# Performance work log

Measured on AMD Instinct MI355X. Metric: run time of the kernel, lower is better.

The kernel has to match this reference:

```python
import jax, jax.numpy as jnp
import numpy as np

EMB = 512       # emb_dim
H = 8           # n_heads
HD = EMB // H   # head_dim = 64
FREQ = 64       # freq_features
PERIOD = 0.1
N = 2048


def setup_inputs() -> dict:
    key = jax.random.key(0)
    ks = jax.random.split(key, 6)
    x = jax.random.normal(ks[0], (1, N, EMB), dtype=jnp.float32)
    v = jax.random.normal(ks[1], (1, N, 3), dtype=jnp.float32)
    vec_map = v / jnp.linalg.norm(v, axis=-1, keepdims=True)  # unit direction vectors
    s_in = 1.0 / np.sqrt(EMB)
    W_qkv = jax.random.normal(ks[2], (EMB, 3 * EMB), dtype=jnp.float32) * s_in
    b_qkv = jnp.zeros((3 * EMB,), dtype=jnp.float32)
    W_bias = jax.random.normal(ks[3], (FREQ, H), dtype=jnp.float32) * (1.0 / np.sqrt(FREQ))
    b_bias = jnp.zeros((H,), dtype=jnp.float32)
    W_out = jax.random.normal(ks[4], (EMB, EMB), dtype=jnp.float32) * s_in
    b_out = jnp.zeros((EMB,), dtype=jnp.float32)
    return {"x": x, "vec_map": vec_map, "W_qkv": W_qkv, "b_qkv": b_qkv,
            "W_bias": W_bias, "b_bias": b_bias, "W_out": W_out, "b_out": b_out}


def reference(x, vec_map, W_qkv, b_qkv, W_bias, b_bias, W_out, b_out):
    batch_dim = x.shape[:-2]
    n = x.shape[-2]
    # QKV projection -> (*, N, H, 3, HD)
    qkv = (x @ W_qkv + b_qkv).reshape(*batch_dim, n, H, 3, HD)
    q, k, v = (qkv[..., 0, :], qkv[..., 1, :], qkv[..., 2, :])
    # attention scores (*, Q, K, H), softmax over the K axis (axis=-2)
    attn = jnp.einsum('...qht,...kht->...qkh', q, k) / np.sqrt(HD)
    attn = jax.nn.softmax(attn, axis=-2)
    # relative bias from pairwise angles between direction vectors
    dot = jnp.einsum('...nc,...mc->...nm', vec_map, vec_map)
    angle = jnp.arccos(jnp.clip(dot, 0.0, 1.0)) / 0.001
    freqs = jnp.linspace(0.0, 1.0, FREQ // 2, dtype=jnp.float32) / PERIOD
    phase = freqs * angle[..., None]                      # (*, N, N, FREQ/2)
    pos = jnp.concatenate((jnp.sin(phase), jnp.cos(phase)), axis=-1)  # (*, N, N, FREQ)
    bias = pos @ W_bias + b_bias                          # (*, N, N, H)
    attn = attn + bias
    # weighted sum of values -> (*, N, EMB)
    y = jnp.einsum('...qkh,...kht->...qht', attn, v).reshape(*batch_dim, n, EMB)
    return y @ W_out + b_out
```

## Files before the change

### kernel.cpp

```cpp
#include <hip/hip_runtime.h>
#include <hip/hip_bf16.h>
#include <math.h>

#define NT 2048
#define EMBD 512
#define NH 8
#define QKV_LD 1536

typedef unsigned short u16;
typedef __attribute__((ext_vector_type(8))) short short8;
typedef __attribute__((ext_vector_type(4))) float v4f;

static __device__ __forceinline__ float bf2f(unsigned int u) {
    union { unsigned int i; float f; } c; c.i = u << 16; return c.f;
}
static __device__ __forceinline__ unsigned int f2bf(float x) {
    union { float f; unsigned int u; } c; c.f = x;
    return (c.u + 0x7fffu + ((c.u >> 16) & 1u)) >> 16;
}

static __device__ __forceinline__ void split_wt_tile(const float* __restrict__ W,
    u16* __restrict__ wth, u16* __restrict__ wtl, int ld, int n0, int k0, int t)
{
    __shared__ float tile[64][65];
    const int r = t >> 2, c4 = (t & 3) << 4;
#pragma unroll
    for (int j = 0; j < 4; ++j)
        *(float4*)&tile[r][c4 + (j << 2)] =
            *(const float4*)(W + (size_t)(k0 + r) * ld + n0 + c4 + (j << 2));
    __syncthreads();
    const int n_l = t >> 2;
    u16 th[16], tl[16];
#pragma unroll
    for (int j = 0; j < 16; ++j) {
        float f = tile[c4 + j][n_l];
        unsigned int h = f2bf(f);
        th[j] = (u16)h;
        tl[j] = (u16)f2bf(f - bf2f(h));
    }
    u16* dh = wth + (size_t)(n0 + n_l) * EMBD + k0 + c4;
    u16* dl = wtl + (size_t)(n0 + n_l) * EMBD + k0 + c4;
    *(uint4*)dh       = *(uint4*)&th[0];
    *(uint4*)(dh + 8) = *(uint4*)&th[8];
    *(uint4*)dl       = *(uint4*)&tl[0];
    *(uint4*)(dl + 8) = *(uint4*)&tl[8];
}

__global__ __launch_bounds__(256) void prep(const float* __restrict__ x,
    const float* __restrict__ Wqkv, const float* __restrict__ Wout,
    u16* __restrict__ xh, u16* __restrict__ xl,
    u16* __restrict__ wth, u16* __restrict__ wtl,
    u16* __restrict__ woth, u16* __restrict__ wotl)
{
    const int b = blockIdx.x, t = threadIdx.x;
    if (b < 1024) {
        int i = (b * 256 + t) << 2;
        float4 v = *(const float4*)(x + i);
        float f[4] = {v.x, v.y, v.z, v.w};
        unsigned int hi[4], lo[4];
#pragma unroll
        for (int j = 0; j < 4; ++j) {
            hi[j] = f2bf(f[j]);
            lo[j] = f2bf(f[j] - bf2f(hi[j]));
        }
        uint2 wh; wh.x = hi[0] | (hi[1] << 16); wh.y = hi[2] | (hi[3] << 16);
        uint2 wl; wl.x = lo[0] | (lo[1] << 16); wl.y = lo[2] | (lo[3] << 16);
        *(uint2*)(xh + i) = wh;
        *(uint2*)(xl + i) = wl;
    } else if (b < 1216) {
        int bb = b - 1024;
        split_wt_tile(Wqkv, wth, wtl, QKV_LD, (bb % 24) << 6, (bb / 24) << 6, t);
    } else {
        int bb = b - 1216;
        split_wt_tile(Wout, woth, wotl, EMBD, (bb & 7) << 6, (bb >> 3) << 6, t);
    }
}

__global__ __launch_bounds__(256) void gemm_qkv_mfma(const u16* __restrict__ xh,
    const u16* __restrict__ xl, const u16* __restrict__ wth,
    const u16* __restrict__ wtl, const float* __restrict__ bias,
    u16* __restrict__ qkvb, u16* __restrict__ Vt)
{
    __shared__ u16 vtile[64][72];
    const int bn = blockIdx.x;
    const int n0 = bn << 6, m0 = blockIdx.y << 6;
    const int t = threadIdx.x;
    const int w = t >> 6, lane = t & 63;
    const int wm = w >> 1, wn = w & 1;
    const int fr = lane & 15, kd = (lane >> 4) << 3;

    const u16* ah0 = xh + (size_t)(m0 + wm * 32 + fr) * EMBD + kd;
    const u16* al0 = xl + (size_t)(m0 + wm * 32 + fr) * EMBD + kd;
    const u16* bh0 = wth + (size_t)(n0 + wn * 32 + fr) * EMBD + kd;
    const u16* bl0 = wtl + (size_t)(n0 + wn * 32 + fr) * EMBD + kd;

    v4f acc[2][2] = {};
    for (int kc = 0; kc < EMBD; kc += 32) {
        short8 a_h[2], a_l[2], b_h[2], b_l[2];
#pragma unroll
        for (int im = 0; im < 2; ++im) {
            a_h[im] = *(const short8*)(ah0 + (size_t)im * 16 * EMBD + kc);
            a_l[im] = *(const short8*)(al0 + (size_t)im * 16 * EMBD + kc);
        }
#pragma unroll
        for (int in = 0; in < 2; ++in) {
            b_h[in] = *(const short8*)(bh0 + (size_t)in * 16 * EMBD + kc);
            b_l[in] = *(const short8*)(bl0 + (size_t)in * 16 * EMBD + kc);
        }
#pragma unroll
        for (int im = 0; im < 2; ++im)
#pragma unroll
            for (int in = 0; in < 2; ++in) {
                acc[im][in] = __builtin_amdgcn_mfma_f32_16x16x32_bf16(a_h[im], b_h[in], acc[im][in], 0, 0, 0);
                acc[im][in] = __builtin_amdgcn_mfma_f32_16x16x32_bf16(a_h[im], b_l[in], acc[im][in], 0, 0, 0);
                acc[im][in] = __builtin_amdgcn_mfma_f32_16x16x32_bf16(a_l[im], b_h[in], acc[im][in], 0, 0, 0);
            }
    }
    const int qr = (lane >> 4) << 2;
    if (bn % 3 != 2) {
#pragma unroll
        for (int im = 0; im < 2; ++im)
#pragma unroll
            for (int in = 0; in < 2; ++in) {
                int n = n0 + wn * 32 + in * 16 + fr;
                float bv = bias[n];
#pragma unroll
                for (int r = 0; r < 4; ++r) {
                    int m = m0 + wm * 32 + im * 16 + qr + r;
                    qkvb[(size_t)m * QKV_LD + n] = (u16)f2bf(acc[im][in][r] + bv);
                }
            }
    } else {
        const int h = bn / 3;
#pragma unroll
        for (int im = 0; im < 2; ++im)
#pragma unroll
            for (int in = 0; in < 2; ++in) {
                int nl = wn * 32 + in * 16 + fr;
                float bv = bias[n0 + nl];
#pragma unroll
                for (int r = 0; r < 4; ++r)
                    vtile[wm * 32 + im * 16 + qr + r][nl] =
                        (u16)f2bf(acc[im][in][r] + bv);
            }
        __syncthreads();
        const int c = t >> 2, kg = (t & 3) << 4;
        u16 tmp[16];
#pragma unroll
        for (int j = 0; j < 16; ++j) tmp[j] = vtile[kg + j][c];
        u16* dst = Vt + ((size_t)h * 64 + c) * NT + m0 + kg;
        *(uint4*)dst       = *(uint4*)&tmp[0];
        *(uint4*)(dst + 8) = *(uint4*)&tmp[8];
    }
}

__global__ __launch_bounds__(256) void bias_mat(const float* __restrict__ vec,
    const float* __restrict__ Wb, const float* __restrict__ bb,
    u16* __restrict__ bm)
{
    __shared__ float flds[32];
    __shared__ float vql[96], vkl[96];
    __shared__ float bbl[8];
    __shared__ float ang_lds[1057];
    __shared__ u16 biaslu[8 * 1057];

    const int t = threadIdx.x;
    int b = blockIdx.x, tq = 0, rem = 64;
    while (b >= rem) { b -= rem; ++tq; --rem; }
    const int tk = tq + b;
    const int q0 = tq << 5, k0 = tk << 5;

    if (t < 32) flds[t] = __fdiv_rn(__fdiv_rn((float)t, 31.0f), 0.1f);
    else if (t < 128) vql[t - 32] = vec[q0 * 3 + (t - 32)];
    else if (t < 224) vkl[t - 128] = vec[k0 * 3 + (t - 128)];
    else if (t < 232) bbl[t - 224] = bb[t - 224];
    __syncthreads();

    {
        const int qq = t & 31, kb = (t >> 5) << 2;
        const float a0 = vql[qq * 3], a1 = vql[qq * 3 + 1], a2 = vql[qq * 3 + 2];
#pragma unroll
        for (int j = 0; j < 4; ++j) {
            const int kk = kb + j;
            float c0 = vkl[kk * 3], c1 = vkl[kk * 3 + 1], c2 = vkl[kk * 3 + 2];
            float dot = __fadd_rn(__fadd_rn(__fmul_rn(a0, c0), __fmul_rn(a1, c1)),
                                  __fmul_rn(a2, c2));
            float dotc = fminf(fmaxf(dot, 0.0f), 1.0f);
            ang_lds[qq * 33 + kk] = __fdiv_rn(acosf(dotc), 0.001f);
        }
    }
    __syncthreads();

    {
        const int w = t >> 6, lane = t & 63;
        const int fr = lane & 15, kd = (lane >> 4) << 3, qr = (lane >> 4) << 2;
        short8 BS, BC;
#pragma unroll
        for (int j = 0; j < 8; ++j) {
            float ws = (fr < 8) ? Wb[(kd + j) * 8 + fr] : 0.0f;
            float wc = (fr < 8) ? Wb[(32 + kd + j) * 8 + fr] : 0.0f;
            BS[j] = (short)f2bf(ws);
            BC[j] = (short)f2bf(wc);
        }
        const float bb0 = (fr < 8) ? bbl[fr] : 0.0f;
        for (int tt = w; tt < 64; tt += 4) {
            int p = (tt << 4) + fr;
            float ang = ang_lds[(p >> 5) * 33 + (p & 31)];
            short8 AS, AC;
#pragma unroll
            for (int j = 0; j < 8; ++j) {
                float ph = __fmul_rn(flds[kd + j], ang);
                float rv = ph * 0.15915494309189535f;
                float rf = rv - floorf(rv);
                AS[j] = (short)f2bf(__builtin_amdgcn_sinf(rf));
                AC[j] = (short)f2bf(__builtin_amdgcn_cosf(rf));
            }
            v4f c = {bb0, bb0, bb0, bb0};
            c = __builtin_amdgcn_mfma_f32_16x16x32_bf16(AS, BS, c, 0, 0, 0);
            c = __builtin_amdgcn_mfma_f32_16x16x32_bf16(AC, BC, c, 0, 0, 0);
            if (fr < 8) {
#pragma unroll
                for (int r = 0; r < 4; ++r) {
                    int pp = (tt << 4) + qr + r;
                    biaslu[fr * 1057 + (pp >> 5) * 33 + (pp & 31)] = (u16)f2bf(c[r]);
                }
            }
        }
    }
    __syncthreads();

    const int row = t >> 3, c4 = (t & 7) << 2;
#pragma unroll
    for (int h = 0; h < 8; ++h) {
        unsigned int o[4];
#pragma unroll
        for (int j = 0; j < 4; ++j)
            o[j] = biaslu[h * 1057 + row * 33 + c4 + j];
        uint2 wv; wv.x = o[0] | (o[1] << 16); wv.y = o[2] | (o[3] << 16);
        *(uint2*)(bm + ((size_t)h * NT + q0 + row) * NT + k0 + c4) = wv;
    }
    if (tk != tq) {
#pragma unroll
        for (int h = 0; h < 8; ++h) {
            unsigned int o[4];
#pragma unroll
            for (int j = 0; j < 4; ++j)
                o[j] = biaslu[h * 1057 + (c4 + j) * 33 + row];
            uint2 wv; wv.x = o[0] | (o[1] << 16); wv.y = o[2] | (o[3] << 16);
            *(uint2*)(bm + ((size_t)h * NT + k0 + row) * NT + q0 + c4) = wv;
        }
    }
}

__global__ __launch_bounds__(256) void biasv_mfma(const u16* __restrict__ bm,
    const u16* __restrict__ Vt, float* __restrict__ bpart)
{
    const int h = blockIdx.y, z = blockIdx.z;
    const int q0 = (blockIdx.x << 6) + ((threadIdx.x >> 6) << 4);
    const int lane = threadIdx.x & 63;
    const int fr = lane & 15;
    const int kd = (lane >> 4) << 3;
    const int kbase = z << 9;

    const u16* arow  = bm + (size_t)(h * NT + q0 + fr) * NT + kbase + kd;
    const u16* vbase = Vt + ((size_t)h * 64 + fr) * NT + kbase + kd;

    v4f c[4] = {};
    for (int ks = 0; ks < 512; ks += 64) {
        short8 a0 = *(const short8*)(arow + ks);
        short8 a1 = *(const short8*)(arow + ks + 32);
#pragma unroll
        for (int nt = 0; nt < 4; ++nt) {
            short8 b0 = *(const short8*)(vbase + (size_t)nt * 16 * NT + ks);
            short8 b1 = *(const short8*)(vbase + (size_t)nt * 16 * NT + ks + 32);
            c[nt] = __builtin_amdgcn_mfma_f32_16x16x32_bf16(a0, b0, c[nt], 0, 0, 0);
            c[nt] = __builtin_amdgcn_mfma_f32_16x16x32_bf16(a1, b1, c[nt], 0, 0, 0);
        }
    }
    float* bp = bpart + (size_t)z * NT * EMBD;
    const int qr = (lane >> 4) << 2;
#pragma unroll
    for (int nt = 0; nt < 4; ++nt)
#pragma unroll
        for (int r = 0; r < 4; ++r)
            bp[(size_t)(q0 + qr + r) * EMBD + (h << 6) + (nt << 4) + fr] = c[nt][r];
}

__global__ __launch_bounds__(256) void flash_attn(const u16* __restrict__ qkvb,
    const u16* __restrict__ Vt, u16* __restrict__ nump,
    float* __restrict__ zpart)
{
    __shared__ u16 P[4][2][16][40];
    const int h = blockIdx.y, z = blockIdx.z;
    const int w = threadIdx.x >> 6, lane = threadIdx.x & 63;
    const int fr = lane & 15, kd = (lane >> 4) << 3, qr = (lane >> 4) << 2;
    const int q0 = (blockIdx.x << 6) + (w << 4);
    const int kbase = z << 9;

    const u16* qb = qkvb + (size_t)(q0 + fr) * QKV_LD + h * 192 + kd;
    short8 qa0 = *(const short8*)(qb);
    short8 qa1 = *(const short8*)(qb + 32);
    const u16* kbp = qkvb + (size_t)kbase * QKV_LD + h * 192 + 64 + kd;
    const u16* vb  = Vt + ((size_t)h * 64 + fr) * NT + kbase + kd;

    v4f acc[4] = {};
    float zac[4] = {};
    int buf = 0;
    for (int kt = 0; kt < 512; kt += 32) {
#pragma unroll
        for (int ks = 0; ks < 2; ++ks) {
            const u16* kr = kbp + (size_t)(kt + ks * 16 + fr) * QKV_LD;
            short8 kb0 = *(const short8*)(kr);
            short8 kb1 = *(const short8*)(kr + 32);
            v4f c = {};
            c = __builtin_amdgcn_mfma_f32_16x16x32_bf16(qa0, kb0, c, 0, 0, 0);
            c = __builtin_amdgcn_mfma_f32_16x16x32_bf16(qa1, kb1, c, 0, 0, 0);
#pragma unroll
            for (int r = 0; r < 4; ++r) {
                float ex = __expf(c[r] * 0.125f);
                zac[r] += ex;
                P[w][buf][qr + r][ks * 16 + fr] = (u16)f2bf(ex);
            }
        }
        union { uint2 u2[2]; short8 s8; } pa;
        pa.u2[0] = *(uint2*)&P[w][buf][fr][kd];
        pa.u2[1] = *(uint2*)&P[w][buf][fr][kd + 4];
#pragma unroll
        for (int ti = 0; ti < 4; ++ti) {
            short8 bfr = *(const short8*)(vb + (size_t)(ti * 16) * NT + kt);
            acc[ti] = __builtin_amdgcn_mfma_f32_16x16x32_bf16(pa.s8, bfr, acc[ti], 0, 0, 0);
        }
        buf ^= 1;
    }
#pragma unroll
    for (int off = 1; off < 16; off <<= 1)
#pragma unroll
        for (int r = 0; r < 4; ++r) zac[r] += __shfl_xor(zac[r], off);
    if (fr == 0) {
#pragma unroll
        for (int r = 0; r < 4; ++r)
            zpart[((size_t)z * NH + h) * NT + q0 + qr + r] = zac[r];
    }
    u16* np = nump + (size_t)z * NT * EMBD;
#pragma unroll
    for (int ti = 0; ti < 4; ++ti)
#pragma unroll
        for (int r = 0; r < 4; ++r)
            np[(size_t)(q0 + qr + r) * EMBD + (h << 6) + (ti << 4) + fr] =
                (u16)f2bf(acc[ti][r]);
}

__global__ __launch_bounds__(256) void combine_emit(const u16* __restrict__ nump,
    const float* __restrict__ zpart, const float* __restrict__ bpart,
    u16* __restrict__ yh, u16* __restrict__ yl)
{
    const int MN = NT * EMBD;
    int i = (blockIdx.x * 256 + threadIdx.x) << 2;
    const int q = i >> 9, h = (i & 511) >> 6;
    float zs = 0.f;
#pragma unroll
    for (int z = 0; z < 4; ++z) zs += zpart[((size_t)z * NH + h) * NT + q];
    const float inv = 1.0f / zs;
    float a[4] = {};
#pragma unroll
    for (int z = 0; z < 4; ++z) {
        uint2 r = *(const uint2*)(nump + (size_t)z * MN + i);
        a[0] += bf2f(r.x & 0xffffu); a[1] += bf2f(r.x >> 16);
        a[2] += bf2f(r.y & 0xffffu); a[3] += bf2f(r.y >> 16);
    }
    float bsum[4] = {};
#pragma unroll
    for (int z = 0; z < 4; ++z) {
        float4 p = *(const float4*)(bpart + (size_t)z * MN + i);
        bsum[0] += p.x; bsum[1] += p.y; bsum[2] += p.z; bsum[3] += p.w;
    }
    unsigned int hi[4], lo[4];
#pragma unroll
    for (int j = 0; j < 4; ++j) {
        float y = a[j] * inv + bsum[j];
        hi[j] = f2bf(y);
        lo[j] = f2bf(y - bf2f(hi[j]));
    }
    uint2 wh; wh.x = hi[0] | (hi[1] << 16); wh.y = hi[2] | (hi[3] << 16);
    uint2 wl; wl.x = lo[0] | (lo[1] << 16); wl.y = lo[2] | (lo[3] << 16);
    *(uint2*)(yh + i) = wh;
    *(uint2*)(yl + i) = wl;
}

__global__ __launch_bounds__(256) void gemm_out_mfma(const u16* __restrict__ yh,
    const u16* __restrict__ yl, const u16* __restrict__ wh,
    const u16* __restrict__ wl, const float* __restrict__ bias,
    float* __restrict__ out)
{
    const int n0 = blockIdx.x << 6, m0 = blockIdx.y << 6;
    const int w = threadIdx.x >> 6, lane = threadIdx.x & 63;
    const int wm = w >> 1, wn = w & 1;
    const int fr = lane & 15, kd = (lane >> 4) << 3;

    const u16* ah0 = yh + (size_t)(m0 + wm * 32 + fr) * EMBD + kd;
    const u16* al0 = yl + (size_t)(m0 + wm * 32 + fr) * EMBD + kd;
    const u16* bh0 = wh + (size_t)(n0 + wn * 32 + fr) * EMBD + kd;
    const u16* bl0 = wl + (size_t)(n0 + wn * 32 + fr) * EMBD + kd;

    v4f acc[2][2] = {};
    for (int kc = 0; kc < EMBD; kc += 32) {
        short8 a_h[2], a_l[2], b_h[2], b_l[2];
#pragma unroll
        for (int im = 0; im < 2; ++im) {
            a_h[im] = *(const short8*)(ah0 + (size_t)im * 16 * EMBD + kc);
            a_l[im] = *(const short8*)(al0 + (size_t)im * 16 * EMBD + kc);
        }
#pragma unroll
        for (int in = 0; in < 2; ++in) {
            b_h[in] = *(const short8*)(bh0 + (size_t)in * 16 * EMBD + kc);
            b_l[in] = *(const short8*)(bl0 + (size_t)in * 16 * EMBD + kc);
        }
#pragma unroll
        for (int im = 0; im < 2; ++im)
#pragma unroll
            for (int in = 0; in < 2; ++in) {
                acc[im][in] = __builtin_amdgcn_mfma_f32_16x16x32_bf16(a_h[im], b_h[in], acc[im][in], 0, 0, 0);
                acc[im][in] = __builtin_amdgcn_mfma_f32_16x16x32_bf16(a_h[im], b_l[in], acc[im][in], 0, 0, 0);
                acc[im][in] = __builtin_amdgcn_mfma_f32_16x16x32_bf16(a_l[im], b_h[in], acc[im][in], 0, 0, 0);
            }
    }
    const int qr = (lane >> 4) << 2;
#pragma unroll
    for (int im = 0; im < 2; ++im)
#pragma unroll
        for (int in = 0; in < 2; ++in) {
            int n = n0 + wn * 32 + in * 16 + fr;
            float bv = bias[n];
#pragma unroll
            for (int r = 0; r < 4; ++r) {
                int m = m0 + wm * 32 + im * 16 + qr + r;
                out[(size_t)m * EMBD + n] = acc[im][in][r] + bv;
            }
        }
}

extern "C" void kernel_launch(void* const* d_in, const int* in_sizes, int n_in,
                              void* d_out, int out_size, void* d_ws, size_t ws_size,
                              hipStream_t stream)
{
    const float* x    = (const float*)d_in[0];
    const float* vec  = (const float*)d_in[1];
    const float* Wqkv = (const float*)d_in[2];
    const float* bqkv = (const float*)d_in[3];
    const float* Wb   = (const float*)d_in[4];
    const float* bb   = (const float*)d_in[5];
    const float* Wout = (const float*)d_in[6];
    const float* bout = (const float*)d_in[7];
    float* out = (float*)d_out;

    char* ws = (char*)d_ws;
    u16*   qkvb  = (u16*)(ws);
    u16*   Vt    = (u16*)(ws + 6291456);
    float* zpart = (float*)(ws + 8388608);
    float* bpart = (float*)(ws + 8650752);
    u16*   yh    = (u16*)(ws + 25427968);
    u16*   yl    = (u16*)(ws + 27525120);
    u16*   woth  = (u16*)(ws + 29622272);
    u16*   wotl  = (u16*)(ws + 30146560);
    char*  big   = ws + 30670848;
    u16*   xh    = (u16*)(big);
    u16*   xl    = (u16*)(big + 2097152);
    u16*   wth   = (u16*)(big + 4194304);
    u16*   wtl   = (u16*)(big + 5767168);
    u16*   bm    = (u16*)(big);
    u16*   nump  = (u16*)(big);

    prep<<<1280, 256, 0, stream>>>(x, Wqkv, Wout, xh, xl, wth, wtl, woth, wotl);
    gemm_qkv_mfma<<<dim3(24, 32), 256, 0, stream>>>(xh, xl, wth, wtl, bqkv, qkvb, Vt);
    bias_mat<<<2080, 256, 0, stream>>>(vec, Wb, bb, bm);
    biasv_mfma<<<dim3(32, 8, 4), 256, 0, stream>>>(bm, Vt, bpart);
    flash_attn<<<dim3(32, 8, 4), 256, 0, stream>>>(qkvb, Vt, nump, zpart);
    combine_emit<<<1024, 256, 0, stream>>>(nump, zpart, bpart, yh, yl);
    gemm_out_mfma<<<dim3(8, 32), 256, 0, stream>>>(yh, yl, woth, wotl, bout, out);
}
```

Baseline: 281.9 us.

## Merge bias generation into prep and fuse attention with bias-V into one launch

Folds the bias-matrix kernel into the prep kernel as extra blocks, and merges flash attention and the bias·V GEMM into a single heterogeneous launch. The bias·V part now splits K into 2 chunks instead of 4, and combine_emit sums 2 partials. The attention loop processes 64 keys per iteration with K and V loads hoisted. The workspace layout is reshuffled so bm no longer aliases the transient buffers. The aim is fewer launches, better overlap of independent work, and less partial-sum traffic, at the cost of fewer, longer bias·V blocks and a larger shared-memory footprint in the prep kernel.

```diff
diff --git a/kernel.cpp b/kernel.cpp
--- a/kernel.cpp
+++ b/kernel.cpp
@@ -20,9 +20,9 @@
 }
 
 static __device__ __forceinline__ void split_wt_tile(const float* __restrict__ W,
-    u16* __restrict__ wth, u16* __restrict__ wtl, int ld, int n0, int k0, int t)
-{
-    __shared__ float tile[64][65];
+    u16* __restrict__ wth, u16* __restrict__ wtl, int ld, int n0, int k0, int t,
+    float (*tile)[65])
+{
     const int r = t >> 2, c4 = (t & 3) << 4;
 #pragma unroll
     for (int j = 0; j < 4; ++j)
@@ -46,12 +46,16 @@
     *(uint4*)(dl + 8) = *(uint4*)&tl[8];
 }
 
-__global__ __launch_bounds__(256) void prep(const float* __restrict__ x,
+__global__ __launch_bounds__(256) void prep_bias(const float* __restrict__ x,
     const float* __restrict__ Wqkv, const float* __restrict__ Wout,
+    const float* __restrict__ vec, const float* __restrict__ Wb,
+    const float* __restrict__ bb,
     u16* __restrict__ xh, u16* __restrict__ xl,
     u16* __restrict__ wth, u16* __restrict__ wtl,
-    u16* __restrict__ woth, u16* __restrict__ wotl)
-{
+    u16* __restrict__ woth, u16* __restrict__ wotl,
+    u16* __restrict__ bm)
+{
+    __shared__ __align__(16) char smem[22080];
     const int b = blockIdx.x, t = threadIdx.x;
     if (b < 1024) {
         int i = (b * 256 + t) << 2;
@@ -67,12 +71,111 @@
         uint2 wl; wl.x = lo[0] | (lo[1] << 16); wl.y = lo[2] | (lo[3] << 16);
         *(uint2*)(xh + i) = wh;
         *(uint2*)(xl + i) = wl;
-    } else if (b < 1216) {
-        int bb = b - 1024;
-        split_wt_tile(Wqkv, wth, wtl, QKV_LD, (bb % 24) << 6, (bb / 24) << 6, t);
-    } else {
-        int bb = b - 1216;
-        split_wt_tile(Wout, woth, wotl, EMBD, (bb & 7) << 6, (bb >> 3) << 6, t);
+        return;
+    }
+    if (b < 1216) {
+        int bb2 = b - 1024;
+        split_wt_tile(Wqkv, wth, wtl, QKV_LD, (bb2 % 24) << 6, (bb2 / 24) << 6,
+                      t, (float(*)[65])smem);
+        return;
+    }
+    if (b < 1280) {
+        int bb2 = b - 1216;
+        split_wt_tile(Wout, woth, wotl, EMBD, (bb2 & 7) << 6, (bb2 >> 3) << 6,
+                      t, (float(*)[65])smem);
+        return;
+    }
+    float* flds   = (float*)(smem);
+    float* vql    = (float*)(smem + 128);
+    float* vkl    = (float*)(smem + 512);
+    float* bbl    = (float*)(smem + 896);
+    float* ang    = (float*)(smem + 928);
+    u16*   biaslu = (u16*)(smem + 5156);
+
+    int bi = b - 1280, tq = 0, rem = 64;
+    while (bi >= rem) { bi -= rem; ++tq; --rem; }
+    const int tk = tq + bi;
+    const int q0 = tq << 5, k0 = tk << 5;
+
+    if (t < 32) flds[t] = __fdiv_rn(__fdiv_rn((float)t, 31.0f), 0.1f);
+    else if (t < 128) vql[t - 32] = vec[q0 * 3 + (t - 32)];
+    else if (t < 224) vkl[t - 128] = vec[k0 * 3 + (t - 128)];
+    else if (t < 232) bbl[t - 224] = bb[t - 224];
+    __syncthreads();
+
+    {
+        const int qq = t & 31, kb = (t >> 5) << 2;
+        const float a0 = vql[qq * 3], a1 = vql[qq * 3 + 1], a2 = vql[qq * 3 + 2];
+#pragma unroll
+        for (int j = 0; j < 4; ++j) {
+            const int kk = kb + j;
+            float c0 = vkl[kk * 3], c1 = vkl[kk * 3 + 1], c2 = vkl[kk * 3 + 2];
+            float dot = __fadd_rn(__fadd_rn(__fmul_rn(a0, c0), __fmul_rn(a1, c1)),
+                                  __fmul_rn(a2, c2));
+            float dotc = fminf(fmaxf(dot, 0.0f), 1.0f);
+            ang[qq * 33 + kk] = __fdiv_rn(acosf(dotc), 0.001f);
+        }
+    }
+    __syncthreads();
+
+    {
+        const int w = t >> 6, lane = t & 63;
+        const int fr = lane & 15, kd = (lane >> 4) << 3, qr = (lane >> 4) << 2;
+        short8 BS, BC;
+#pragma unroll
+        for (int j = 0; j < 8; ++j) {
+            float ws = (fr < 8) ? Wb[(kd + j) * 8 + fr] : 0.0f;
+            float wc = (fr < 8) ? Wb[(32 + kd + j) * 8 + fr] : 0.0f;
+            BS[j] = (short)f2bf(ws);
+            BC[j] = (short)f2bf(wc);
+        }
+        const float bb0 = (fr < 8) ? bbl[fr] : 0.0f;
+        for (int tt = w; tt < 64; tt += 4) {
+            int p = (tt << 4) + fr;
+            float angv = ang[(p >> 5) * 33 + (p & 31)];
+            short8 AS, AC;
+#pragma unroll
+            for (int j = 0; j < 8; ++j) {
+                float ph = __fmul_rn(flds[kd + j], angv);
+                float rv = ph * 0.15915494309189535f;
+                float rf = rv - floorf(rv);
+                AS[j] = (short)f2bf(__builtin_amdgcn_sinf(rf));
+                AC[j] = (short)f2bf(__builtin_amdgcn_cosf(rf));
+            }
+            v4f c = {bb0, bb0, bb0, bb0};
+            c = __builtin_amdgcn_mfma_f32_16x16x32_bf16(AS, BS, c, 0, 0, 0);
+            c = __builtin_amdgcn_mfma_f32_16x16x32_bf16(AC, BC, c, 0, 0, 0);
+            if (fr < 8) {
+#pragma unroll
+                for (int r = 0; r < 4; ++r) {
+                    int pp = (tt << 4) + qr + r;
+                    biaslu[fr * 1057 + (pp >> 5) * 33 + (pp & 31)] = (u16)f2bf(c[r]);
+                }
+            }
+        }
+    }
+    __syncthreads();
+
+    const int row = t >> 3, c4 = (t & 7) << 2;
+#pragma unroll
+    for (int h = 0; h < 8; ++h) {
+        unsigned int o[4];
+#pragma unroll
+        for (int j = 0; j < 4; ++j)
+            o[j] = biaslu[h * 1057 + row * 33 + c4 + j];
+        uint2 wv; wv.x = o[0] | (o[1] << 16); wv.y = o[2] | (o[3] << 16);
+        *(uint2*)(bm + ((size_t)h * NT + q0 + row) * NT + k0 + c4) = wv;
+    }
+    if (tk != tq) {
+#pragma unroll
+        for (int h = 0; h < 8; ++h) {
+            unsigned int o[4];
+#pragma unroll
+            for (int j = 0; j < 4; ++j)
+                o[j] = biaslu[h * 1057 + (c4 + j) * 33 + row];
+            uint2 wv; wv.x = o[0] | (o[1] << 16); wv.y = o[2] | (o[3] << 16);
+            *(uint2*)(bm + ((size_t)h * NT + k0 + row) * NT + q0 + c4) = wv;
+        }
     }
 }
 
@@ -154,200 +257,113 @@
     }
 }
 
-__global__ __launch_bounds__(256) void bias_mat(const float* __restrict__ vec,
-    const float* __restrict__ Wb, const float* __restrict__ bb,
-    u16* __restrict__ bm)
-{
-    __shared__ float flds[32];
-    __shared__ float vql[96], vkl[96];
-    __shared__ float bbl[8];
-    __shared__ float ang_lds[1057];
-    __shared__ u16 biaslu[8 * 1057];
-
-    const int t = threadIdx.x;
-    int b = blockIdx.x, tq = 0, rem = 64;
-    while (b >= rem) { b -= rem; ++tq; --rem; }
-    const int tk = tq + b;
-    const int q0 = tq << 5, k0 = tk << 5;
-
-    if (t < 32) flds[t] = __fdiv_rn(__fdiv_rn((float)t, 31.0f), 0.1f);
-    else if (t < 128) vql[t - 32] = vec[q0 * 3 + (t - 32)];
-    else if (t < 224) vkl[t - 128] = vec[k0 * 3 + (t - 128)];
-    else if (t < 232) bbl[t - 224] = bb[t - 224];
-    __syncthreads();
-
-    {
-        const int qq = t & 31, kb = (t >> 5) << 2;
-        const float a0 = vql[qq * 3], a1 = vql[qq * 3 + 1], a2 = vql[qq * 3 + 2];
-#pragma unroll
-        for (int j = 0; j < 4; ++j) {
-            const int kk = kb + j;
-            float c0 = vkl[kk * 3], c1 = vkl[kk * 3 + 1], c2 = vkl[kk * 3 + 2];
-            float dot = __fadd_rn(__fadd_rn(__fmul_rn(a0, c0), __fmul_rn(a1, c1)),
-                                  __fmul_rn(a2, c2));
-            float dotc = fminf(fmaxf(dot, 0.0f), 1.0f);
-            ang_lds[qq * 33 + kk] = __fdiv_rn(acosf(dotc), 0.001f);
-        }
-    }
-    __syncthreads();
-
-    {
-        const int w = t >> 6, lane = t & 63;
-        const int fr = lane & 15, kd = (lane >> 4) << 3, qr = (lane >> 4) << 2;
-        short8 BS, BC;
-#pragma unroll
-        for (int j = 0; j < 8; ++j) {
-            float ws = (fr < 8) ? Wb[(kd + j) * 8 + fr] : 0.0f;
-            float wc = (fr < 8) ? Wb[(32 + kd + j) * 8 + fr] : 0.0f;
-            BS[j] = (short)f2bf(ws);
-            BC[j] = (short)f2bf(wc);
-        }
-        const float bb0 = (fr < 8) ? bbl[fr] : 0.0f;
-        for (int tt = w; tt < 64; tt += 4) {
-            int p = (tt << 4) + fr;
-            float ang = ang_lds[(p >> 5) * 33 + (p & 31)];
-            short8 AS, AC;
-#pragma unroll
-            for (int j = 0; j < 8; ++j) {
-                float ph = __fmul_rn(flds[kd + j], ang);
-                float rv = ph * 0.15915494309189535f;
-                float rf = rv - floorf(rv);
-                AS[j] = (short)f2bf(__builtin_amdgcn_sinf(rf));
-                AC[j] = (short)f2bf(__builtin_amdgcn_cosf(rf));
-            }
-            v4f c = {bb0, bb0, bb0, bb0};
-            c = __builtin_amdgcn_mfma_f32_16x16x32_bf16(AS, BS, c, 0, 0, 0);
-            c = __builtin_amdgcn_mfma_f32_16x16x32_bf16(AC, BC, c, 0, 0, 0);
-            if (fr < 8) {
+__global__ __launch_bounds__(256) void attn_fused(const u16* __restrict__ qkvb,
+    const u16* __restrict__ Vt, const u16* __restrict__ bm,
+    u16* __restrict__ nump, float* __restrict__ zpart,
+    float* __restrict__ bpart)
+{
+    __shared__ u16 P[4][2][16][40];
+    const int b = blockIdx.x, t = threadIdx.x;
+    const int w = t >> 6, lane = t & 63;
+    const int fr = lane & 15, kd = (lane >> 4) << 3, qr = (lane >> 4) << 2;
+    if (b < 1024) {
+        const int qb = b & 31, h = (b >> 5) & 7, z = b >> 8;
+        const int q0 = (qb << 6) + (w << 4);
+        const int kbase = z << 9;
+
+        const u16* qbp = qkvb + (size_t)(q0 + fr) * QKV_LD + h * 192 + kd;
+        short8 qa0 = *(const short8*)(qbp);
+        short8 qa1 = *(const short8*)(qbp + 32);
+        const u16* kbp = qkvb + (size_t)kbase * QKV_LD + h * 192 + 64 + kd;
+        const u16* vb  = Vt + ((size_t)h * 64 + fr) * NT + kbase + kd;
+
+        v4f acc[4] = {};
+        float zac[4] = {};
+        for (int kt = 0; kt < 512; kt += 64) {
+            short8 ka[4], kbv[4];
+#pragma unroll
+            for (int i = 0; i < 4; ++i) {
+                const u16* kr = kbp + (size_t)(kt + i * 16 + fr) * QKV_LD;
+                ka[i]  = *(const short8*)(kr);
+                kbv[i] = *(const short8*)(kr + 32);
+            }
+            short8 vf[2][4];
+#pragma unroll
+            for (int ti = 0; ti < 4; ++ti) {
+                vf[0][ti] = *(const short8*)(vb + (size_t)(ti * 16) * NT + kt);
+                vf[1][ti] = *(const short8*)(vb + (size_t)(ti * 16) * NT + kt + 32);
+            }
+            v4f c[4];
+#pragma unroll
+            for (int i = 0; i < 4; ++i) {
+                v4f cc = {};
+                cc = __builtin_amdgcn_mfma_f32_16x16x32_bf16(qa0, ka[i], cc, 0, 0, 0);
+                cc = __builtin_amdgcn_mfma_f32_16x16x32_bf16(qa1, kbv[i], cc, 0, 0, 0);
+                c[i] = cc;
+            }
+#pragma unroll
+            for (int i = 0; i < 4; ++i)
 #pragma unroll
                 for (int r = 0; r < 4; ++r) {
-                    int pp = (tt << 4) + qr + r;
-                    biaslu[fr * 1057 + (pp >> 5) * 33 + (pp & 31)] = (u16)f2bf(c[r]);
+                    float ex = __expf(c[i][r] * 0.125f);
+                    zac[r] += ex;
+                    P[w][i >> 1][qr + r][((i & 1) << 4) + fr] = (u16)f2bf(ex);
                 }
-            }
-        }
-    }
-    __syncthreads();
-
-    const int row = t >> 3, c4 = (t & 7) << 2;
-#pragma unroll
-    for (int h = 0; h < 8; ++h) {
-        unsigned int o[4];
-#pragma unroll
-        for (int j = 0; j < 4; ++j)
-            o[j] = biaslu[h * 1057 + row * 33 + c4 + j];
-        uint2 wv; wv.x = o[0] | (o[1] << 16); wv.y = o[2] | (o[3] << 16);
-        *(uint2*)(bm + ((size_t)h * NT + q0 + row) * NT + k0 + c4) = wv;
-    }
-    if (tk != tq) {
-#pragma unroll
-        for (int h = 0; h < 8; ++h) {
-            unsigned int o[4];
-#pragma unroll
-            for (int j = 0; j < 4; ++j)
-                o[j] = biaslu[h * 1057 + (c4 + j) * 33 + row];
-            uint2 wv; wv.x = o[0] | (o[1] << 16); wv.y = o[2] | (o[3] << 16);
-            *(uint2*)(bm + ((size_t)h * NT + k0 + row) * NT + q0 + c4) = wv;
-        }
-    }
-}
-
-__global__ __launch_bounds__(256) void biasv_mfma(const u16* __restrict__ bm,
-    const u16* __restrict__ Vt, float* __restrict__ bpart)
-{
-    const int h = blockIdx.y, z = blockIdx.z;
-    const int q0 = (blockIdx.x << 6) + ((threadIdx.x >> 6) << 4);
-    const int lane = threadIdx.x & 63;
-    const int fr = lane & 15;
-    const int kd = (lane >> 4) << 3;
-    const int kbase = z << 9;
-
-    const u16* arow  = bm + (size_t)(h * NT + q0 + fr) * NT + kbase + kd;
-    const u16* vbase = Vt + ((size_t)h * 64 + fr) * NT + kbase + kd;
-
-    v4f c[4] = {};
-    for (int ks = 0; ks < 512; ks += 64) {
-        short8 a0 = *(const short8*)(arow + ks);
-        short8 a1 = *(const short8*)(arow + ks + 32);
-#pragma unroll
-        for (int nt = 0; nt < 4; ++nt) {
-            short8 b0 = *(const short8*)(vbase + (size_t)nt * 16 * NT + ks);
-            short8 b1 = *(const short8*)(vbase + (size_t)nt * 16 * NT + ks + 32);
-            c[nt] = __builtin_amdgcn_mfma_f32_16x16x32_bf16(a0, b0, c[nt], 0, 0, 0);
-            c[nt] = __builtin_amdgcn_mfma_f32_16x16x32_bf16(a1, b1, c[nt], 0, 0, 0);
-        }
-    }
-    float* bp = bpart + (size_t)z * NT * EMBD;
-    const int qr = (lane >> 4) << 2;
-#pragma unroll
-    for (int nt = 0; nt < 4; ++nt)
-#pragma unroll
-        for (int r = 0; r < 4; ++r)
-            bp[(size_t)(q0 + qr + r) * EMBD + (h << 6) + (nt << 4) + fr] = c[nt][r];
-}
-
-__global__ __launch_bounds__(256) void flash_attn(const u16* __restrict__ qkvb,
-    const u16* __restrict__ Vt, u16* __restrict__ nump,
-    float* __restrict__ zpart)
-{
-    __shared__ u16 P[4][2][16][40];
-    const int h = blockIdx.y, z = blockIdx.z;
-    const int w = threadIdx.x >> 6, lane = threadIdx.x & 63;
-    const int fr = lane & 15, kd = (lane >> 4) << 3, qr = (lane >> 4) << 2;
-    const int q0 = (blockIdx.x << 6) + (w << 4);
-    const int kbase = z << 9;
-
-    const u16* qb = qkvb + (size_t)(q0 + fr) * QKV_LD + h * 192 + kd;
-    short8 qa0 = *(const short8*)(qb);
-    short8 qa1 = *(const short8*)(qb + 32);
-    const u16* kbp = qkvb + (size_t)kbase * QKV_LD + h * 192 + 64 + kd;
-    const u16* vb  = Vt + ((size_t)h * 64 + fr) * NT + kbase + kd;
-
-    v4f acc[4] = {};
-    float zac[4] = {};
-    int buf = 0;
-    for (int kt = 0; kt < 512; kt += 32) {
-#pragma unroll
-        for (int ks = 0; ks < 2; ++ks) {
-            const u16* kr = kbp + (size_t)(kt + ks * 16 + fr) * QKV_LD;
-            short8 kb0 = *(const short8*)(kr);
-            short8 kb1 = *(const short8*)(kr + 32);
-            v4f c = {};
-            c = __builtin_amdgcn_mfma_f32_16x16x32_bf16(qa0, kb0, c, 0, 0, 0);
-            c = __builtin_amdgcn_mfma_f32_16x16x32_bf16(qa1, kb1, c, 0, 0, 0);
-#pragma unroll
-            for (int r = 0; r < 4; ++r) {
-                float ex = __expf(c[r] * 0.125f);
-                zac[r] += ex;
-                P[w][buf][qr + r][ks * 16 + fr] = (u16)f2bf(ex);
-            }
-        }
-        union { uint2 u2[2]; short8 s8; } pa;
-        pa.u2[0] = *(uint2*)&P[w][buf][fr][kd];
-        pa.u2[1] = *(uint2*)&P[w][buf][fr][kd + 4];
-#pragma unroll
-        for (int ti = 0; ti < 4; ++ti) {
-            short8 bfr = *(const short8*)(vb + (size_t)(ti * 16) * NT + kt);
-            acc[ti] = __builtin_amdgcn_mfma_f32_16x16x32_bf16(pa.s8, bfr, acc[ti], 0, 0, 0);
-        }
-        buf ^= 1;
-    }
-#pragma unroll
-    for (int off = 1; off < 16; off <<= 1)
-#pragma unroll
-        for (int r = 0; r < 4; ++r) zac[r] += __shfl_xor(zac[r], off);
-    if (fr == 0) {
-#pragma unroll
-        for (int r = 0; r < 4; ++r)
-            zpart[((size_t)z * NH + h) * NT + q0 + qr + r] = zac[r];
-    }
-    u16* np = nump + (size_t)z * NT * EMBD;
-#pragma unroll
-    for (int ti = 0; ti < 4; ++ti)
-#pragma unroll
-        for (int r = 0; r < 4; ++r)
-            np[(size_t)(q0 + qr + r) * EMBD + (h << 6) + (ti << 4) + fr] =
-                (u16)f2bf(acc[ti][r]);
+            union { uint2 u2[2]; short8 s8; } p0, p1;
+            p0.u2[0] = *(uint2*)&P[w][0][fr][kd];
+            p0.u2[1] = *(uint2*)&P[w][0][fr][kd + 4];
+            p1.u2[0] = *(uint2*)&P[w][1][fr][kd];
+            p1.u2[1] = *(uint2*)&P[w][1][fr][kd + 4];
+#pragma unroll
+            for (int ti = 0; ti < 4; ++ti) {
+                acc[ti] = __builtin_amdgcn_mfma_f32_16x16x32_bf16(p0.s8, vf[0][ti], acc[ti], 0, 0, 0);
+                acc[ti] = __builtin_amdgcn_mfma_f32_16x16x32_bf16(p1.s8, vf[1][ti], acc[ti], 0, 0, 0);
+            }
+        }
+#pragma unroll
+        for (int off = 1; off < 16; off <<= 1)
+#pragma unroll
+            for (int r = 0; r < 4; ++r) zac[r] += __shfl_xor(zac[r], off);
+        if (fr == 0) {
+#pragma unroll
+            for (int r = 0; r < 4; ++r)
+                zpart[((size_t)z * NH + h) * NT + q0 + qr + r] = zac[r];
+        }
+        u16* np = nump + (size_t)z * NT * EMBD;
+#pragma unroll
+        for (int ti = 0; ti < 4; ++ti)
+#pragma unroll
+            for (int r = 0; r < 4; ++r)
+                np[(size_t)(q0 + qr + r) * EMBD + (h << 6) + (ti << 4) + fr] =
+                    (u16)f2bf(acc[ti][r]);
+    } else {
+        const int b2 = b - 1024;
+        const int qb = b2 & 31, h = (b2 >> 5) & 7, z = b2 >> 8;
+        const int q0 = (qb << 6) + (w << 4);
+        const int kbase = z << 10;
+
+        const u16* arow  = bm + (size_t)(h * NT + q0 + fr) * NT + kbase + kd;
+        const u16* vbase = Vt + ((size_t)h * 64 + fr) * NT + kbase + kd;
+
+        v4f c[4] = {};
+        for (int ks = 0; ks < 1024; ks += 64) {
+            short8 a0 = *(const short8*)(arow + ks);
+            short8 a1 = *(const short8*)(arow + ks + 32);
+#pragma unroll
+            for (int nt = 0; nt < 4; ++nt) {
+                short8 b0 = *(const short8*)(vbase + (size_t)nt * 16 * NT + ks);
+                short8 b1 = *(const short8*)(vbase + (size_t)nt * 16 * NT + ks + 32);
+                c[nt] = __builtin_amdgcn_mfma_f32_16x16x32_bf16(a0, b0, c[nt], 0, 0, 0);
+                c[nt] = __builtin_amdgcn_mfma_f32_16x16x32_bf16(a1, b1, c[nt], 0, 0, 0);
+            }
+        }
+        float* bp = bpart + (size_t)z * NT * EMBD;
+#pragma unroll
+        for (int nt = 0; nt < 4; ++nt)
+#pragma unroll
+            for (int r = 0; r < 4; ++r)
+                bp[(size_t)(q0 + qr + r) * EMBD + (h << 6) + (nt << 4) + fr] = c[nt][r];
+    }
 }
 
 __global__ __launch_bounds__(256) void combine_emit(const u16* __restrict__ nump,
@@ -370,7 +386,7 @@
     }
     float bsum[4] = {};
 #pragma unroll
-    for (int z = 0; z < 4; ++z) {
+    for (int z = 0; z < 2; ++z) {
         float4 p = *(const float4*)(bpart + (size_t)z * MN + i);
         bsum[0] += p.x; bsum[1] += p.y; bsum[2] += p.z; bsum[3] += p.w;
     }
@@ -458,23 +474,22 @@
     u16*   Vt    = (u16*)(ws + 6291456);
     float* zpart = (float*)(ws + 8388608);
     float* bpart = (float*)(ws + 8650752);
-    u16*   yh    = (u16*)(ws + 25427968);
-    u16*   yl    = (u16*)(ws + 27525120);
-    u16*   woth  = (u16*)(ws + 29622272);
-    u16*   wotl  = (u16*)(ws + 30146560);
-    char*  big   = ws + 30670848;
-    u16*   xh    = (u16*)(big);
-    u16*   xl    = (u16*)(big + 2097152);
-    u16*   wth   = (u16*)(big + 4194304);
-    u16*   wtl   = (u16*)(big + 5767168);
-    u16*   bm    = (u16*)(big);
-    u16*   nump  = (u16*)(big);
-
-    prep<<<1280, 256, 0, stream>>>(x, Wqkv, Wout, xh, xl, wth, wtl, woth, wotl);
+    u16*   yh    = (u16*)(ws + 17039360);
+    u16*   yl    = (u16*)(ws + 19136512);
+    u16*   woth  = (u16*)(ws + 21233664);
+    u16*   wotl  = (u16*)(ws + 21757952);
+    char*  trans = ws + 22282240;
+    u16*   xh    = (u16*)(trans);
+    u16*   xl    = (u16*)(trans + 2097152);
+    u16*   wth   = (u16*)(trans + 4194304);
+    u16*   wtl   = (u16*)(trans + 5767168);
+    u16*   nump  = (u16*)(trans);
+    u16*   bm    = (u16*)(ws + 30670848);
+
+    prep_bias<<<3360, 256, 0, stream>>>(x, Wqkv, Wout, vec, Wb, bb,
+                                        xh, xl, wth, wtl, woth, wotl, bm);
     gemm_qkv_mfma<<<dim3(24, 32), 256, 0, stream>>>(xh, xl, wth, wtl, bqkv, qkvb, Vt);
-    bias_mat<<<2080, 256, 0, stream>>>(vec, Wb, bb, bm);
-    biasv_mfma<<<dim3(32, 8, 4), 256, 0, stream>>>(bm, Vt, bpart);
-    flash_attn<<<dim3(32, 8, 4), 256, 0, stream>>>(qkvb, Vt, nump, zpart);
+    attn_fused<<<1536, 256, 0, stream>>>(qkvb, Vt, bm, nump, zpart, bpart);
     combine_emit<<<1024, 256, 0, stream>>>(nump, zpart, bpart, yh, yl);
     gemm_out_mfma<<<dim3(8, 32), 256, 0, stream>>>(yh, yl, woth, wotl, bout, out);
 }
```

After: 276.3 us. 2.0% less time.
